# Performance work log

Hardware: AMD Instinct MI355X
Metric: run time of the kernel (lower is better)

Reference implementation:

```python
import jax, jax.numpy as jnp
import numpy as np

WS = 8  # window size (module uses window_sizes as a scalar)


def setup_inputs() -> dict:
    key = jax.random.key(0)
    ks = jax.random.split(key, 4)
    b, c, h, w = 4, 128, 256, 256
    x = jax.random.normal(ks[0], (b, c, h, w), jnp.float32)
    w_qkv = jax.random.normal(ks[1], (3 * c, c), jnp.float32) * (1.0 / np.sqrt(c))
    w_dw = jax.random.normal(ks[2], (3 * c, 1, 3, 3), jnp.float32) * (1.0 / 3.0)
    w_proj = jax.random.normal(ks[3], (c, c), jnp.float32) * (1.0 / np.sqrt(c))
    temperature = jnp.ones((1, 1, 1), jnp.float32)
    return {"x": x, "w_qkv": w_qkv, "w_dw": w_dw, "w_proj": w_proj,
            "temperature": temperature}


def _window(t, ws):
    # b c (h dh) (w dw) -> b (h w) (dh dw) c
    b, c, H, W = t.shape
    t = t.reshape(b, c, H // ws, ws, W // ws, ws)
    return t.transpose(0, 2, 4, 3, 5, 1).reshape(b, (H // ws) * (W // ws), ws * ws, c)


def _unwindow(t, ws, H, W):
    # b (h w) (dh dw) c -> b c (h dh) (w dw)
    b = t.shape[0]
    c = t.shape[-1]
    t = t.reshape(b, H // ws, W // ws, ws, ws, c)
    return t.transpose(0, 5, 1, 3, 2, 4).reshape(b, c, H, W)


def reference(x, w_qkv, w_dw, w_proj, temperature):
    b, c, H, W = x.shape
    ws = WS
    sh = -ws // 2  # = -(ws//2) for even ws, matching torch.roll shifts
    x_ = jnp.roll(x, (sh, sh), axis=(2, 3))
    # 1x1 conv c -> 3c
    qkv = jnp.einsum('oc,bchw->bohw', w_qkv, x_)
    # depthwise 3x3, padding 1
    qkv = jax.lax.conv_general_dilated(
        qkv, w_dw, window_strides=(1, 1), padding=[(1, 1), (1, 1)],
        dimension_numbers=('NCHW', 'OIHW', 'NCHW'), feature_group_count=3 * c)
    q, k, v = jnp.split(qkv, 3, axis=1)
    q = _window(q, ws)  # [b, nW, ws*ws, c]
    k = _window(k, ws)
    v = _window(v, ws)
    # L2-normalize along channel dim (torch F.normalize, eps=1e-12)
    q = q / jnp.maximum(jnp.linalg.norm(q, axis=-1, keepdims=True), 1e-12)
    k = k / jnp.maximum(jnp.linalg.norm(k, axis=-1, keepdims=True), 1e-12)
    # channel-wise attention: [b, nW, c, c]
    attn = jnp.einsum('bnpc,bnpd->bncd', q, k) * temperature.reshape(())
    attn = jax.nn.relu(attn)
    out = jnp.einsum('bnpc,bncd->bnpd', v, attn)  # [b, nW, ws*ws, c]
    out = _unwindow(out, ws, H, W)
    out = jnp.roll(out, (ws // 2, ws // 2), axis=(2, 3))
    y = jnp.einsum('oc,bchw->bohw', w_proj, out)
    return (y, attn)
```

## Files before the change

### kernel.cpp

```cpp
#include <hip/hip_runtime.h>
#include <hip/hip_bf16.h>

constexpr int NB = 4;
constexpr int CC = 128;
constexpr int HW = 65536;

using bf16x8 = __attribute__((ext_vector_type(8))) short;
using f32x4  = __attribute__((ext_vector_type(4))) float;

__device__ __forceinline__ unsigned short f2bf(float f) {
  unsigned u = __builtin_bit_cast(unsigned, f);
  u += 0x7FFFu + ((u >> 16) & 1u);
  return (unsigned short)(u >> 16);
}
__device__ __forceinline__ float bf2f(unsigned short s) {
  return __builtin_bit_cast(float, (unsigned)s << 16);
}

__device__ __forceinline__ void halo_decomp(int idx, int& ch, int& r, int& c) {
  ch = idx / 30;
  int rem = idx - ch * 30;
  r = rem / 3;
  c = rem - r * 3;
}
__device__ __forceinline__ uint4 halo_load_one(const __hip_bfloat16* __restrict__ base,
                                               int ih0, int iw0, int idx) {
  int ch, r, c;
  halo_decomp(idx, ch, r, c);
  int ii = ih0 - 1 + r, j0 = iw0 - 8 + c * 8;
  uint4 v = {0u, 0u, 0u, 0u};
  if ((unsigned)ii < 256u && (unsigned)j0 <= 248u)
    v = *(const uint4*)(base + (((size_t)ch) << 16) + (ii << 8) + j0);
  return v;
}
__device__ __forceinline__ void halo_store_one(unsigned short* __restrict__ halo,
                                               int idx, uint4 v) {
  int ch, r, c;
  halo_decomp(idx, ch, r, c);
  unsigned short* hrow = halo + ch * 168 + r * 16;
  if (c == 1) *(uint4*)hrow = v;
  else if (c == 0) hrow[9] = (unsigned short)(v.w >> 16);
  else hrow[8] = (unsigned short)(v.x & 0xFFFFu);
}

__device__ __forceinline__ void dw_row(const unsigned short* __restrict__ halo,
                                       const float* __restrict__ wd,
                                       int ch, int pr, float* __restrict__ outv) {
#pragma unroll
  for (int pc = 0; pc < 8; ++pc) outv[pc] = 0.f;
#pragma unroll
  for (int kr = 0; kr < 3; ++kr) {
    const unsigned short* hrow = halo + ch * 168 + (pr + kr) * 16;
    uint4 rw = *(const uint4*)hrow;
    float rv[10];
    rv[0] = bf2f((unsigned short)(rw.x & 0xFFFFu));
    rv[1] = bf2f((unsigned short)(rw.x >> 16));
    rv[2] = bf2f((unsigned short)(rw.y & 0xFFFFu));
    rv[3] = bf2f((unsigned short)(rw.y >> 16));
    rv[4] = bf2f((unsigned short)(rw.z & 0xFFFFu));
    rv[5] = bf2f((unsigned short)(rw.z >> 16));
    rv[6] = bf2f((unsigned short)(rw.w & 0xFFFFu));
    rv[7] = bf2f((unsigned short)(rw.w >> 16));
    rv[8] = bf2f(hrow[8]);
    rv[9] = bf2f(hrow[9]);
#pragma unroll
    for (int s = 0; s < 3; ++s) {
      float wv = wd[kr * 3 + s];
#pragma unroll
      for (int pc = 0; pc < 8; ++pc) {
        int m = pc + s - 1;
        float xv = (m < 0) ? rv[9] : rv[m];
        outv[pc] = fmaf(wv, xv, outv[pc]);
      }
    }
  }
}

__global__ __launch_bounds__(256) void k_qkv_mfma(const float* __restrict__ x,
                                                  const float* __restrict__ wq,
                                                  __hip_bfloat16* __restrict__ qkv) {
  __shared__ unsigned short x_s[128 * 136];

  int blk = blockIdx.x;
  int b = blk >> 9, i = (blk >> 1) & 255, jh = blk & 1;
  int j0 = jh << 7;
  int si = (i + 4) & 255;
  int t = threadIdx.x;

  {
    int c0 = (t & 63) << 1;
    int jb = (t >> 6) << 5;
    const float* xr0 = x + (((size_t)(b * CC + c0)) << 16) + (si << 8);
    const float* xr1 = xr0 + HW;
#pragma unroll
    for (int u = 0; u < 8; ++u) {
      int jj = jb + (u << 2);
      int sj = j0 + jj + 4;
      float v0[4], v1[4];
      if (sj + 3 <= 255) {
        *(float4*)v0 = *(const float4*)(xr0 + sj);
        *(float4*)v1 = *(const float4*)(xr1 + sj);
      } else {
#pragma unroll
        for (int e = 0; e < 4; ++e) {
          int s = (sj + e) & 255;
          v0[e] = xr0[s];
          v1[e] = xr1[s];
        }
      }
#pragma unroll
      for (int e = 0; e < 4; ++e) {
        unsigned pk = (unsigned)f2bf(v0[e]) | ((unsigned)f2bf(v1[e]) << 16);
        *(unsigned*)&x_s[(jj + e) * 136 + c0] = pk;
      }
    }
  }
  __syncthreads();

  int w = t >> 6;
  int lane = t & 63;
  int col = lane & 15;
  int kg = lane >> 4;

#pragma unroll 1
  for (int oi = 0; oi < 3; ++oi) {
    int m0 = oi * 128 + w * 32;
    bf16x8 afr[2][4];
#pragma unroll
    for (int mt = 0; mt < 2; ++mt) {
      const float* wr = wq + (m0 + mt * 16 + col) * CC + kg * 8;
#pragma unroll
      for (int ks = 0; ks < 4; ++ks) {
        float wa[4], wb[4];
        *(float4*)wa = *(const float4*)(wr + ks * 32);
        *(float4*)wb = *(const float4*)(wr + ks * 32 + 4);
        bf16x8 f;
#pragma unroll
        for (int e = 0; e < 4; ++e) {
          f[e] = (short)f2bf(wa[e]);
          f[e + 4] = (short)f2bf(wb[e]);
        }
        afr[mt][ks] = f;
      }
    }
#pragma unroll 1
    for (int n = 0; n < 8; ++n) {
      int px = n * 16 + col;
      f32x4 acc0 = {0.f, 0.f, 0.f, 0.f};
      f32x4 acc1 = {0.f, 0.f, 0.f, 0.f};
#pragma unroll
      for (int ks = 0; ks < 4; ++ks) {
        bf16x8 bfr = *(const bf16x8*)&x_s[px * 136 + ks * 32 + kg * 8];
        acc0 = __builtin_amdgcn_mfma_f32_16x16x32_bf16(afr[0][ks], bfr, acc0, 0, 0, 0);
        acc1 = __builtin_amdgcn_mfma_f32_16x16x32_bf16(afr[1][ks], bfr, acc1, 0, 0, 0);
      }
      int j = j0 + n * 16 + col;
#pragma unroll
      for (int r = 0; r < 4; ++r) {
        int och0 = m0 + kg * 4 + r;
        int och1 = m0 + 16 + kg * 4 + r;
        int g0 = och0 >> 7, c0 = och0 & 127;
        int g1 = och1 >> 7, c1 = och1 & 127;
        qkv[(((size_t)((g0 * NB + b) * CC + c0)) << 16) + (i << 8) + j] =
            __float2bfloat16(acc0[r]);
        qkv[(((size_t)((g1 * NB + b) * CC + c1)) << 16) + (i << 8) + j] =
            __float2bfloat16(acc1[r]);
      }
    }
  }
}

__global__ __launch_bounds__(256, 2) void k_fused(const __hip_bfloat16* __restrict__ qkv,
                                                  const float* __restrict__ wdw,
                                                  const float* __restrict__ temp_p,
                                                  const float* __restrict__ wp,
                                                  float* __restrict__ attn_out,
                                                  float* __restrict__ y) {
  __shared__ unsigned short halo_s[128 * 168];
  __shared__ unsigned short q_t[128][72];
  __shared__ unsigned short k_t[128][72];
  __shared__ float sumsq_s[2][64];

  int bid = blockIdx.x;
  int blk = ((bid & 7) << 9) + (bid >> 3);
  int b = blk >> 10, n = blk & 1023;
  int ih0 = (n >> 5) << 3, iw0 = (n & 31) << 3;
  int t = threadIdx.x;
  int ch_l = t & 15, grp = t >> 4;
  int pr = grp & 7, contrib = grp >> 3;
  float tau = temp_p[0];
  const __hip_bfloat16* qbase = qkv + (((size_t)(b * CC)) << 16);
  const __hip_bfloat16* kbase = qkv + (((size_t)((NB + b) * CC)) << 16);
  const __hip_bfloat16* vbase = qkv + (((size_t)((2 * NB + b) * CC)) << 16);

#pragma unroll
  for (int it = 0; it < 15; ++it) {
    int idx = it * 256 + t;
    halo_store_one(halo_s, idx, halo_load_one(qbase, ih0, iw0, idx));
  }
  __syncthreads();

  uint4 kpre[15];
#pragma unroll
  for (int it = 0; it < 15; ++it)
    kpre[it] = halo_load_one(kbase, ih0, iw0, it * 256 + t);

  float outv[4][8];
  float ssq[8];
#pragma unroll
  for (int pc = 0; pc < 8; ++pc) ssq[pc] = 0.f;
#pragma unroll
  for (int it = 0; it < 4; ++it) {
    int ch = ((contrib + 2 * it) << 4) + ch_l;
    float wd[9];
#pragma unroll
    for (int kk = 0; kk < 9; ++kk) wd[kk] = wdw[ch * 9 + kk];
    dw_row(halo_s, wd, ch, pr, outv[it]);
#pragma unroll
    for (int pc = 0; pc < 8; ++pc) ssq[pc] = fmaf(outv[it][pc], outv[it][pc], ssq[pc]);
  }
#pragma unroll
  for (int pc = 0; pc < 8; ++pc) {
    float s = ssq[pc];
    s += __shfl_xor(s, 1);
    s += __shfl_xor(s, 2);
    s += __shfl_xor(s, 4);
    s += __shfl_xor(s, 8);
    ssq[pc] = s;
  }
  if (ch_l == 0) {
#pragma unroll
    for (int pc = 0; pc < 8; ++pc) sumsq_s[contrib][pr * 8 + pc] = ssq[pc];
  }
  __syncthreads();

#pragma unroll
  for (int it = 0; it < 15; ++it) halo_store_one(halo_s, it * 256 + t, kpre[it]);
  {
    float psv[8];
#pragma unroll
    for (int pc = 0; pc < 8; ++pc) {
      float s = sumsq_s[0][pr * 8 + pc] + sumsq_s[1][pr * 8 + pc];
      psv[pc] = 1.f / fmaxf(sqrtf(s), 1e-12f);
    }
#pragma unroll
    for (int it = 0; it < 4; ++it) {
      int ch = ((contrib + 2 * it) << 4) + ch_l;
      unsigned short o8[8];
#pragma unroll
      for (int pc = 0; pc < 8; ++pc) o8[pc] = f2bf(outv[it][pc] * psv[pc]);
      *(uint4*)&q_t[ch][pr * 8] = *(const uint4*)o8;
    }
  }
  __syncthreads();

#pragma unroll
  for (int pc = 0; pc < 8; ++pc) ssq[pc] = 0.f;
#pragma unroll
  for (int it = 0; it < 4; ++it) {
    int ch = ((contrib + 2 * it) << 4) + ch_l;
    float wd[9];
#pragma unroll
    for (int kk = 0; kk < 9; ++kk) wd[kk] = wdw[(CC + ch) * 9 + kk];
    dw_row(halo_s, wd, ch, pr, outv[it]);
#pragma unroll
    for (int pc = 0; pc < 8; ++pc) ssq[pc] = fmaf(outv[it][pc], outv[it][pc], ssq[pc]);
  }
#pragma unroll
  for (int pc = 0; pc < 8; ++pc) {
    float s = ssq[pc];
    s += __shfl_xor(s, 1);
    s += __shfl_xor(s, 2);
    s += __shfl_xor(s, 4);
    s += __shfl_xor(s, 8);
    ssq[pc] = s;
  }
  if (ch_l == 0) {
#pragma unroll
    for (int pc = 0; pc < 8; ++pc) sumsq_s[contrib][pr * 8 + pc] = ssq[pc];
  }
  __syncthreads();

  {
    float psv[8];
#pragma unroll
    for (int pc = 0; pc < 8; ++pc) {
      float s = sumsq_s[0][pr * 8 + pc] + sumsq_s[1][pr * 8 + pc];
      psv[pc] = tau / fmaxf(sqrtf(s), 1e-12f);
    }
#pragma unroll
    for (int it = 0; it < 4; ++it) {
      int ch = ((contrib + 2 * it) << 4) + ch_l;
      unsigned short o8[8];
#pragma unroll
      for (int pc = 0; pc < 8; ++pc) o8[pc] = f2bf(outv[it][pc] * psv[pc]);
      *(uint4*)&k_t[ch][pr * 8] = *(const uint4*)o8;
    }
  }
  __syncthreads();

  uint4 vpre[15];
#pragma unroll
  for (int it = 0; it < 15; ++it)
    vpre[it] = halo_load_one(vbase, ih0, iw0, it * 256 + t);

  int wv = t >> 6, lane = t & 63;
  int col = lane & 15, kg = lane >> 4;
  int c0 = wv * 32;
  f32x4 pa0[8], pa1[8];
  {
    bf16x8 afr[2][2];
#pragma unroll
    for (int mt = 0; mt < 2; ++mt)
#pragma unroll
      for (int ks = 0; ks < 2; ++ks)
        afr[mt][ks] = *(const bf16x8*)&q_t[c0 + mt * 16 + col][ks * 32 + kg * 8];
    float* ao = attn_out + ((size_t)blk << 14);
#pragma unroll
    for (int dt = 0; dt < 8; ++dt) {
      bf16x8 b0 = *(const bf16x8*)&k_t[dt * 16 + col][kg * 8];
      bf16x8 b1 = *(const bf16x8*)&k_t[dt * 16 + col][32 + kg * 8];
      f32x4 a0 = {0.f, 0.f, 0.f, 0.f};
      f32x4 a1 = {0.f, 0.f, 0.f, 0.f};
      a0 = __builtin_amdgcn_mfma_f32_16x16x32_bf16(afr[0][0], b0, a0, 0, 0, 0);
      a0 = __builtin_amdgcn_mfma_f32_16x16x32_bf16(afr[0][1], b1, a0, 0, 0, 0);
      a1 = __builtin_amdgcn_mfma_f32_16x16x32_bf16(afr[1][0], b0, a1, 0, 0, 0);
      a1 = __builtin_amdgcn_mfma_f32_16x16x32_bf16(afr[1][1], b1, a1, 0, 0, 0);
#pragma unroll
      for (int r = 0; r < 4; ++r) {
        a0[r] = fmaxf(a0[r], 0.f);
        a1[r] = fmaxf(a1[r], 0.f);
        ao[((c0 + kg * 4 + r) << 7) + dt * 16 + col] = a0[r];
        ao[((c0 + 16 + kg * 4 + r) << 7) + dt * 16 + col] = a1[r];
      }
      pa0[dt] = a0;
      pa1[dt] = a1;
    }
  }
  __syncthreads();

#pragma unroll
  for (int it = 0; it < 15; ++it) halo_store_one(halo_s, it * 256 + t, vpre[it]);
  __syncthreads();

  unsigned short (*v_t)[136] = (unsigned short (*)[136])&q_t[0][0];
#pragma unroll
  for (int it = 0; it < 4; ++it) {
    int ch = ((contrib + 2 * it) << 4) + ch_l;
    float wd[9];
#pragma unroll
    for (int kk = 0; kk < 9; ++kk) wd[kk] = wdw[(2 * CC + ch) * 9 + kk];
    float vo[8];
    dw_row(halo_s, wd, ch, pr, vo);
#pragma unroll
    for (int pc = 0; pc < 8; ++pc) v_t[pr * 8 + pc][ch] = f2bf(vo[pc]);
  }
  __syncthreads();

  unsigned short (*a_t)[136] = (unsigned short (*)[136])halo_s;
#pragma unroll
  for (int dt = 0; dt < 8; ++dt)
#pragma unroll
    for (int r = 0; r < 4; ++r) {
      a_t[dt * 16 + col][c0 + kg * 4 + r] = f2bf(pa0[dt][r]);
      a_t[dt * 16 + col][c0 + 16 + kg * 4 + r] = f2bf(pa1[dt][r]);
    }
  __syncthreads();

  f32x4 pacc[8];
#pragma unroll
  for (int dt = 0; dt < 8; ++dt) pacc[dt] = {0.f, 0.f, 0.f, 0.f};
#pragma unroll
  for (int ks = 0; ks < 4; ++ks) {
    bf16x8 va = *(const bf16x8*)&v_t[wv * 16 + col][ks * 32 + kg * 8];
#pragma unroll
    for (int dt = 0; dt < 8; ++dt) {
      bf16x8 bf = *(const bf16x8*)&a_t[dt * 16 + col][ks * 32 + kg * 8];
      pacc[dt] = __builtin_amdgcn_mfma_f32_16x16x32_bf16(va, bf, pacc[dt], 0, 0, 0);
    }
  }
  __syncthreads();

  unsigned short (*po_t)[136] = (unsigned short (*)[136])halo_s;
#pragma unroll
  for (int dt = 0; dt < 8; ++dt)
#pragma unroll
    for (int r = 0; r < 4; ++r)
      po_t[wv * 16 + kg * 4 + r][dt * 16 + col] = f2bf(pacc[dt][r]);
  __syncthreads();

  {
    int p = wv * 16 + col;
    bf16x8 bfr[4];
#pragma unroll
    for (int ks = 0; ks < 4; ++ks)
      bfr[ks] = *(const bf16x8*)&po_t[p][ks * 32 + kg * 8];
    int i_f = (((n >> 5) << 3) + (p >> 3) + 4) & 255;
    int j_f = (((n & 31) << 3) + (p & 7) + 4) & 255;
    float* yp = y + (((size_t)b * CC) << 16) + (i_f << 8) + j_f;
#pragma unroll
    for (int mt = 0; mt < 8; ++mt) {
      bf16x8 afr[4];
      const float* wr = wp + (mt * 16 + col) * CC + kg * 8;
#pragma unroll
      for (int ks = 0; ks < 4; ++ks) {
        float wa[4], wb[4];
        *(float4*)wa = *(const float4*)(wr + ks * 32);
        *(float4*)wb = *(const float4*)(wr + ks * 32 + 4);
        bf16x8 f;
#pragma unroll
        for (int e = 0; e < 4; ++e) {
          f[e] = (short)f2bf(wa[e]);
          f[e + 4] = (short)f2bf(wb[e]);
        }
        afr[ks] = f;
      }
      f32x4 acc = {0.f, 0.f, 0.f, 0.f};
#pragma unroll
      for (int ks = 0; ks < 4; ++ks)
        acc = __builtin_amdgcn_mfma_f32_16x16x32_bf16(afr[ks], bfr[ks], acc, 0, 0, 0);
#pragma unroll
      for (int r = 0; r < 4; ++r) {
        int och = mt * 16 + kg * 4 + r;
        yp[(size_t)och << 16] = acc[r];
      }
    }
  }
}

extern "C" void kernel_launch(void* const* d_in, const int* in_sizes, int n_in,
                              void* d_out, int out_size, void* d_ws, size_t ws_size,
                              hipStream_t stream) {
  const float* x = (const float*)d_in[0];
  const float* w_qkv = (const float*)d_in[1];
  const float* w_dw = (const float*)d_in[2];
  const float* w_proj = (const float*)d_in[3];
  const float* temp = (const float*)d_in[4];
  float* y = (float*)d_out;
  float* attn = (float*)d_out + (size_t)NB * CC * HW;

  __hip_bfloat16* qkv = (__hip_bfloat16*)d_ws;

  k_qkv_mfma<<<2048, 256, 0, stream>>>(x, w_qkv, qkv);
  k_fused<<<4096, 256, 0, stream>>>(qkv, w_dw, temp, w_proj, attn, y);
}
```

Measured before the change: 646.6 us.

## Halve halo staging, swizzle LDS tiles, and raise occupancy to three blocks

The fused window-attention kernel now stages the depthwise-conv halo in 64-channel halves instead of all 128 channels. It overlaps the next half's global prefetch with the current half's depthwise compute and splits the V·attn MFMA loop into two K-halves. Shared memory is shrunk and the transposed q/k/v/attn tiles use XOR-swizzled layouts to avoid bank conflicts. Both kernels get launch bounds of 3 blocks per CU. In exchange the kernel needs more barriers and has a tighter register budget, which risks spills.

Result: slower. 965.7 us (+49.4%).

```diff
diff --git a/kernel.cpp b/kernel.cpp
--- a/kernel.cpp
+++ b/kernel.cpp
@@ -17,26 +17,25 @@
   return __builtin_bit_cast(float, (unsigned)s << 16);
 }
 
-__device__ __forceinline__ void halo_decomp(int idx, int& ch, int& r, int& c) {
-  ch = idx / 30;
+__device__ __forceinline__ int swz128(int row, int b) { return row * 128 + (b ^ ((row & 7) << 4)); }
+__device__ __forceinline__ int swz256(int row, int b) { return row * 256 + (b ^ ((row & 15) << 4)); }
+
+__device__ __forceinline__ uint4 hload(const __hip_bfloat16* __restrict__ base,
+                                       int ih0, int iw0, int idx) {
+  int ch = idx / 30;
   int rem = idx - ch * 30;
-  r = rem / 3;
-  c = rem - r * 3;
-}
-__device__ __forceinline__ uint4 halo_load_one(const __hip_bfloat16* __restrict__ base,
-                                               int ih0, int iw0, int idx) {
-  int ch, r, c;
-  halo_decomp(idx, ch, r, c);
+  int r = rem / 3, c = rem - r * 3;
   int ii = ih0 - 1 + r, j0 = iw0 - 8 + c * 8;
   uint4 v = {0u, 0u, 0u, 0u};
-  if ((unsigned)ii < 256u && (unsigned)j0 <= 248u)
+  if (idx < 1920 && (unsigned)ii < 256u && (unsigned)j0 <= 248u)
     v = *(const uint4*)(base + (((size_t)ch) << 16) + (ii << 8) + j0);
   return v;
 }
-__device__ __forceinline__ void halo_store_one(unsigned short* __restrict__ halo,
-                                               int idx, uint4 v) {
-  int ch, r, c;
-  halo_decomp(idx, ch, r, c);
+__device__ __forceinline__ void hstore(unsigned short* __restrict__ halo, int idx, uint4 v) {
+  if (idx >= 1920) return;
+  int ch = idx / 30;
+  int rem = idx - ch * 30;
+  int r = rem / 3, c = rem - r * 3;
   unsigned short* hrow = halo + ch * 168 + r * 16;
   if (c == 1) *(uint4*)hrow = v;
   else if (c == 0) hrow[9] = (unsigned short)(v.w >> 16);
@@ -45,12 +44,12 @@
 
 __device__ __forceinline__ void dw_row(const unsigned short* __restrict__ halo,
                                        const float* __restrict__ wd,
-                                       int ch, int pr, float* __restrict__ outv) {
+                                       int chl, int pr, float* __restrict__ outv) {
 #pragma unroll
   for (int pc = 0; pc < 8; ++pc) outv[pc] = 0.f;
 #pragma unroll
   for (int kr = 0; kr < 3; ++kr) {
-    const unsigned short* hrow = halo + ch * 168 + (pr + kr) * 16;
+    const unsigned short* hrow = halo + chl * 168 + (pr + kr) * 16;
     uint4 rw = *(const uint4*)hrow;
     float rv[10];
     rv[0] = bf2f((unsigned short)(rw.x & 0xFFFFu));
@@ -76,9 +75,30 @@
   }
 }
 
-__global__ __launch_bounds__(256) void k_qkv_mfma(const float* __restrict__ x,
-                                                  const float* __restrict__ wq,
-                                                  __hip_bfloat16* __restrict__ qkv) {
+template <bool SQ>
+__device__ __forceinline__ void dw_half(const unsigned short* __restrict__ halo,
+                                        const float* __restrict__ wdw_g,
+                                        int g0, int ch_l, int pr, int half,
+                                        float (*outv)[8], float* __restrict__ ssq) {
+#pragma unroll
+  for (int it = 0; it < 2; ++it) {
+    int chl = (g0 + 2 * it) * 16 + ch_l;
+    int chf = half * 64 + chl;
+    float wd[9];
+#pragma unroll
+    for (int kk = 0; kk < 9; ++kk) wd[kk] = wdw_g[chf * 9 + kk];
+    dw_row(halo, wd, chl, pr, outv[it]);
+    if (SQ) {
+#pragma unroll
+      for (int pc = 0; pc < 8; ++pc)
+        ssq[pc] = fmaf(outv[it][pc], outv[it][pc], ssq[pc]);
+    }
+  }
+}
+
+__global__ __launch_bounds__(256, 3) void k_qkv_mfma(const float* __restrict__ x,
+                                                     const float* __restrict__ wq,
+                                                     __hip_bfloat16* __restrict__ qkv) {
   __shared__ unsigned short x_s[128 * 136];
 
   int blk = blockIdx.x;
@@ -170,142 +190,116 @@
   }
 }
 
-__global__ __launch_bounds__(256, 2) void k_fused(const __hip_bfloat16* __restrict__ qkv,
+__global__ __launch_bounds__(256, 3) void k_fused(const __hip_bfloat16* __restrict__ qkv,
                                                   const float* __restrict__ wdw,
                                                   const float* __restrict__ temp_p,
                                                   const float* __restrict__ wp,
                                                   float* __restrict__ attn_out,
                                                   float* __restrict__ y) {
-  __shared__ unsigned short halo_s[128 * 168];
-  __shared__ unsigned short q_t[128][72];
-  __shared__ unsigned short k_t[128][72];
-  __shared__ float sumsq_s[2][64];
+  __shared__ __align__(16) char smem[54272];
+  unsigned short* halo = (unsigned short*)smem;
+  char* RB = smem + 21504;
+  char* RC = smem + 21504 + 16384;
 
   int bid = blockIdx.x;
   int blk = ((bid & 7) << 9) + (bid >> 3);
   int b = blk >> 10, n = blk & 1023;
   int ih0 = (n >> 5) << 3, iw0 = (n & 31) << 3;
   int t = threadIdx.x;
-  int ch_l = t & 15, grp = t >> 4;
-  int pr = grp & 7, contrib = grp >> 3;
+  int ch_l = t & 15;
+  int wv = t >> 6, lane = t & 63;
+  int col = lane & 15, kg = lane >> 4;
+  int giw = (t >> 4) & 3;
+  int pr = 2 * wv + (giw & 1);
+  int g0 = giw >> 1;
   float tau = temp_p[0];
-  const __hip_bfloat16* qbase = qkv + (((size_t)(b * CC)) << 16);
-  const __hip_bfloat16* kbase = qkv + (((size_t)((NB + b) * CC)) << 16);
-  const __hip_bfloat16* vbase = qkv + (((size_t)((2 * NB + b) * CC)) << 16);
-
-#pragma unroll
-  for (int it = 0; it < 15; ++it) {
-    int idx = it * 256 + t;
-    halo_store_one(halo_s, idx, halo_load_one(qbase, ih0, iw0, idx));
-  }
-  __syncthreads();
-
-  uint4 kpre[15];
-#pragma unroll
-  for (int it = 0; it < 15; ++it)
-    kpre[it] = halo_load_one(kbase, ih0, iw0, it * 256 + t);
-
+  const __hip_bfloat16* qb = qkv + (((size_t)(b * CC)) << 16);
+  const __hip_bfloat16* kb = qb + (((size_t)(NB * CC)) << 16);
+  const __hip_bfloat16* vb = qb + (((size_t)(2 * NB * CC)) << 16);
+  const size_t HALF = ((size_t)64) << 16;
+
+  uint4 pre[8];
   float outv[4][8];
   float ssq[8];
+
+#pragma unroll
+  for (int it = 0; it < 8; ++it) {
+    int idx = it * 256 + t;
+    hstore(halo, idx, hload(qb, ih0, iw0, idx));
+  }
+  __syncthreads();
+#pragma unroll
+  for (int it = 0; it < 8; ++it) pre[it] = hload(qb + HALF, ih0, iw0, it * 256 + t);
 #pragma unroll
   for (int pc = 0; pc < 8; ++pc) ssq[pc] = 0.f;
-#pragma unroll
-  for (int it = 0; it < 4; ++it) {
-    int ch = ((contrib + 2 * it) << 4) + ch_l;
-    float wd[9];
-#pragma unroll
-    for (int kk = 0; kk < 9; ++kk) wd[kk] = wdw[ch * 9 + kk];
-    dw_row(halo_s, wd, ch, pr, outv[it]);
-#pragma unroll
-    for (int pc = 0; pc < 8; ++pc) ssq[pc] = fmaf(outv[it][pc], outv[it][pc], ssq[pc]);
-  }
-#pragma unroll
-  for (int pc = 0; pc < 8; ++pc) {
-    float s = ssq[pc];
-    s += __shfl_xor(s, 1);
-    s += __shfl_xor(s, 2);
-    s += __shfl_xor(s, 4);
-    s += __shfl_xor(s, 8);
-    ssq[pc] = s;
-  }
-  if (ch_l == 0) {
-#pragma unroll
-    for (int pc = 0; pc < 8; ++pc) sumsq_s[contrib][pr * 8 + pc] = ssq[pc];
-  }
-  __syncthreads();
-
-#pragma unroll
-  for (int it = 0; it < 15; ++it) halo_store_one(halo_s, it * 256 + t, kpre[it]);
+  dw_half<true>(halo, wdw, g0, ch_l, pr, 0, &outv[0], ssq);
+  __syncthreads();
+#pragma unroll
+  for (int it = 0; it < 8; ++it) hstore(halo, it * 256 + t, pre[it]);
+  __syncthreads();
+#pragma unroll
+  for (int it = 0; it < 8; ++it) pre[it] = hload(kb, ih0, iw0, it * 256 + t);
+  dw_half<true>(halo, wdw, g0, ch_l, pr, 1, &outv[2], ssq);
   {
     float psv[8];
 #pragma unroll
     for (int pc = 0; pc < 8; ++pc) {
-      float s = sumsq_s[0][pr * 8 + pc] + sumsq_s[1][pr * 8 + pc];
+      float s = ssq[pc];
+      s += __shfl_xor(s, 1); s += __shfl_xor(s, 2);
+      s += __shfl_xor(s, 4); s += __shfl_xor(s, 8);
+      s += __shfl_xor(s, 32);
       psv[pc] = 1.f / fmaxf(sqrtf(s), 1e-12f);
     }
 #pragma unroll
-    for (int it = 0; it < 4; ++it) {
-      int ch = ((contrib + 2 * it) << 4) + ch_l;
+    for (int tk = 0; tk < 4; ++tk) {
+      int chf = (tk >> 1) * 64 + (g0 + 2 * (tk & 1)) * 16 + ch_l;
       unsigned short o8[8];
 #pragma unroll
-      for (int pc = 0; pc < 8; ++pc) o8[pc] = f2bf(outv[it][pc] * psv[pc]);
-      *(uint4*)&q_t[ch][pr * 8] = *(const uint4*)o8;
-    }
-  }
-  __syncthreads();
-
+      for (int pc = 0; pc < 8; ++pc) o8[pc] = f2bf(outv[tk][pc] * psv[pc]);
+      *(uint4*)(RB + swz128(chf, pr * 16)) = *(const uint4*)o8;
+    }
+  }
+  __syncthreads();
+#pragma unroll
+  for (int it = 0; it < 8; ++it) hstore(halo, it * 256 + t, pre[it]);
+  __syncthreads();
+#pragma unroll
+  for (int it = 0; it < 8; ++it) pre[it] = hload(kb + HALF, ih0, iw0, it * 256 + t);
 #pragma unroll
   for (int pc = 0; pc < 8; ++pc) ssq[pc] = 0.f;
-#pragma unroll
-  for (int it = 0; it < 4; ++it) {
-    int ch = ((contrib + 2 * it) << 4) + ch_l;
-    float wd[9];
-#pragma unroll
-    for (int kk = 0; kk < 9; ++kk) wd[kk] = wdw[(CC + ch) * 9 + kk];
-    dw_row(halo_s, wd, ch, pr, outv[it]);
-#pragma unroll
-    for (int pc = 0; pc < 8; ++pc) ssq[pc] = fmaf(outv[it][pc], outv[it][pc], ssq[pc]);
-  }
-#pragma unroll
-  for (int pc = 0; pc < 8; ++pc) {
-    float s = ssq[pc];
-    s += __shfl_xor(s, 1);
-    s += __shfl_xor(s, 2);
-    s += __shfl_xor(s, 4);
-    s += __shfl_xor(s, 8);
-    ssq[pc] = s;
-  }
-  if (ch_l == 0) {
-#pragma unroll
-    for (int pc = 0; pc < 8; ++pc) sumsq_s[contrib][pr * 8 + pc] = ssq[pc];
-  }
-  __syncthreads();
-
+  dw_half<true>(halo, wdw + CC * 9, g0, ch_l, pr, 0, &outv[0], ssq);
+  __syncthreads();
+#pragma unroll
+  for (int it = 0; it < 8; ++it) hstore(halo, it * 256 + t, pre[it]);
+  __syncthreads();
+#pragma unroll
+  for (int it = 0; it < 8; ++it) pre[it] = hload(vb, ih0, iw0, it * 256 + t);
+  dw_half<true>(halo, wdw + CC * 9, g0, ch_l, pr, 1, &outv[2], ssq);
   {
     float psv[8];
 #pragma unroll
     for (int pc = 0; pc < 8; ++pc) {
-      float s = sumsq_s[0][pr * 8 + pc] + sumsq_s[1][pr * 8 + pc];
+      float s = ssq[pc];
+      s += __shfl_xor(s, 1); s += __shfl_xor(s, 2);
+      s += __shfl_xor(s, 4); s += __shfl_xor(s, 8);
+      s += __shfl_xor(s, 32);
       psv[pc] = tau / fmaxf(sqrtf(s), 1e-12f);
     }
 #pragma unroll
-    for (int it = 0; it < 4; ++it) {
-      int ch = ((contrib + 2 * it) << 4) + ch_l;
+    for (int tk = 0; tk < 4; ++tk) {
+      int chf = (tk >> 1) * 64 + (g0 + 2 * (tk & 1)) * 16 + ch_l;
       unsigned short o8[8];
 #pragma unroll
-      for (int pc = 0; pc < 8; ++pc) o8[pc] = f2bf(outv[it][pc] * psv[pc]);
-      *(uint4*)&k_t[ch][pr * 8] = *(const uint4*)o8;
-    }
-  }
-  __syncthreads();
-
-  uint4 vpre[15];
-#pragma unroll
-  for (int it = 0; it < 15; ++it)
-    vpre[it] = halo_load_one(vbase, ih0, iw0, it * 256 + t);
-
-  int wv = t >> 6, lane = t & 63;
-  int col = lane & 15, kg = lane >> 4;
+      for (int pc = 0; pc < 8; ++pc) o8[pc] = f2bf(outv[tk][pc] * psv[pc]);
+      *(uint4*)(RC + swz128(chf, pr * 16)) = *(const uint4*)o8;
+    }
+  }
+  __syncthreads();
+#pragma unroll
+  for (int it = 0; it < 8; ++it) hstore(halo, it * 256 + t, pre[it]);
+  __syncthreads();
+#pragma unroll
+  for (int it = 0; it < 8; ++it) pre[it] = hload(vb + HALF, ih0, iw0, it * 256 + t);
   int c0 = wv * 32;
   f32x4 pa0[8], pa1[8];
   {
@@ -314,12 +308,12 @@
     for (int mt = 0; mt < 2; ++mt)
 #pragma unroll
       for (int ks = 0; ks < 2; ++ks)
-        afr[mt][ks] = *(const bf16x8*)&q_t[c0 + mt * 16 + col][ks * 32 + kg * 8];
+        afr[mt][ks] = *(const bf16x8*)(RB + swz128(c0 + mt * 16 + col, ks * 64 + kg * 16));
     float* ao = attn_out + ((size_t)blk << 14);
 #pragma unroll
     for (int dt = 0; dt < 8; ++dt) {
-      bf16x8 b0 = *(const bf16x8*)&k_t[dt * 16 + col][kg * 8];
-      bf16x8 b1 = *(const bf16x8*)&k_t[dt * 16 + col][32 + kg * 8];
+      bf16x8 b0 = *(const bf16x8*)(RC + swz128(dt * 16 + col, kg * 16));
+      bf16x8 b1 = *(const bf16x8*)(RC + swz128(dt * 16 + col, 64 + kg * 16));
       f32x4 a0 = {0.f, 0.f, 0.f, 0.f};
       f32x4 a1 = {0.f, 0.f, 0.f, 0.f};
       a0 = __builtin_amdgcn_mfma_f32_16x16x32_bf16(afr[0][0], b0, a0, 0, 0, 0);
@@ -338,63 +332,89 @@
     }
   }
   __syncthreads();
-
-#pragma unroll
-  for (int it = 0; it < 15; ++it) halo_store_one(halo_s, it * 256 + t, vpre[it]);
-  __syncthreads();
-
-  unsigned short (*v_t)[136] = (unsigned short (*)[136])&q_t[0][0];
-#pragma unroll
-  for (int it = 0; it < 4; ++it) {
-    int ch = ((contrib + 2 * it) << 4) + ch_l;
-    float wd[9];
-#pragma unroll
-    for (int kk = 0; kk < 9; ++kk) wd[kk] = wdw[(2 * CC + ch) * 9 + kk];
-    float vo[8];
-    dw_row(halo_s, wd, ch, pr, vo);
-#pragma unroll
-    for (int pc = 0; pc < 8; ++pc) v_t[pr * 8 + pc][ch] = f2bf(vo[pc]);
-  }
-  __syncthreads();
-
-  unsigned short (*a_t)[136] = (unsigned short (*)[136])halo_s;
+  {
+    float vo[2][8];
+    dw_half<false>(halo, wdw + 2 * CC * 9, g0, ch_l, pr, 0, vo, nullptr);
+#pragma unroll
+    for (int it = 0; it < 2; ++it) {
+      int chf = (g0 + 2 * it) * 16 + ch_l;
+#pragma unroll
+      for (int pc = 0; pc < 8; ++pc)
+        *(unsigned short*)(RB + swz256(pr * 8 + pc, chf * 2)) = f2bf(vo[it][pc]);
+    }
+  }
+  if (wv < 2) {
+#pragma unroll
+    for (int dt = 0; dt < 8; ++dt)
+#pragma unroll
+      for (int r = 0; r < 4; ++r) {
+        int d = dt * 16 + col;
+        *(unsigned short*)(RC + swz128(d, (c0 + kg * 4 + r) * 2)) = f2bf(pa0[dt][r]);
+        *(unsigned short*)(RC + swz128(d, (c0 + 16 + kg * 4 + r) * 2)) = f2bf(pa1[dt][r]);
+      }
+  }
+  __syncthreads();
+#pragma unroll
+  for (int it = 0; it < 8; ++it) hstore(halo, it * 256 + t, pre[it]);
+  f32x4 pacc[8];
+#pragma unroll
+  for (int dt = 0; dt < 8; ++dt) pacc[dt] = {0.f, 0.f, 0.f, 0.f};
+#pragma unroll
+  for (int ks = 0; ks < 2; ++ks) {
+    bf16x8 va = *(const bf16x8*)(RB + swz256(wv * 16 + col, ks * 64 + kg * 16));
+#pragma unroll
+    for (int dt = 0; dt < 8; ++dt) {
+      bf16x8 bf = *(const bf16x8*)(RC + swz128(dt * 16 + col, (ks & 1) * 64 + kg * 16));
+      pacc[dt] = __builtin_amdgcn_mfma_f32_16x16x32_bf16(va, bf, pacc[dt], 0, 0, 0);
+    }
+  }
+  __syncthreads();
+  {
+    float vo[2][8];
+    dw_half<false>(halo, wdw + 2 * CC * 9, g0, ch_l, pr, 1, vo, nullptr);
+#pragma unroll
+    for (int it = 0; it < 2; ++it) {
+      int chf = 64 + (g0 + 2 * it) * 16 + ch_l;
+#pragma unroll
+      for (int pc = 0; pc < 8; ++pc)
+        *(unsigned short*)(RB + swz256(pr * 8 + pc, chf * 2)) = f2bf(vo[it][pc]);
+    }
+  }
+  if (wv >= 2) {
+    int cl0 = c0 - 64;
+#pragma unroll
+    for (int dt = 0; dt < 8; ++dt)
+#pragma unroll
+      for (int r = 0; r < 4; ++r) {
+        int d = dt * 16 + col;
+        *(unsigned short*)(RC + swz128(d, (cl0 + kg * 4 + r) * 2)) = f2bf(pa0[dt][r]);
+        *(unsigned short*)(RC + swz128(d, (cl0 + 16 + kg * 4 + r) * 2)) = f2bf(pa1[dt][r]);
+      }
+  }
+  __syncthreads();
+#pragma unroll
+  for (int ks = 2; ks < 4; ++ks) {
+    bf16x8 va = *(const bf16x8*)(RB + swz256(wv * 16 + col, ks * 64 + kg * 16));
+#pragma unroll
+    for (int dt = 0; dt < 8; ++dt) {
+      bf16x8 bf = *(const bf16x8*)(RC + swz128(dt * 16 + col, (ks & 1) * 64 + kg * 16));
+      pacc[dt] = __builtin_amdgcn_mfma_f32_16x16x32_bf16(va, bf, pacc[dt], 0, 0, 0);
+    }
+  }
+  __syncthreads();
 #pragma unroll
   for (int dt = 0; dt < 8; ++dt)
 #pragma unroll
-    for (int r = 0; r < 4; ++r) {
-      a_t[dt * 16 + col][c0 + kg * 4 + r] = f2bf(pa0[dt][r]);
-      a_t[dt * 16 + col][c0 + 16 + kg * 4 + r] = f2bf(pa1[dt][r]);
-    }
-  __syncthreads();
-
-  f32x4 pacc[8];
-#pragma unroll
-  for (int dt = 0; dt < 8; ++dt) pacc[dt] = {0.f, 0.f, 0.f, 0.f};
-#pragma unroll
-  for (int ks = 0; ks < 4; ++ks) {
-    bf16x8 va = *(const bf16x8*)&v_t[wv * 16 + col][ks * 32 + kg * 8];
-#pragma unroll
-    for (int dt = 0; dt < 8; ++dt) {
-      bf16x8 bf = *(const bf16x8*)&a_t[dt * 16 + col][ks * 32 + kg * 8];
-      pacc[dt] = __builtin_amdgcn_mfma_f32_16x16x32_bf16(va, bf, pacc[dt], 0, 0, 0);
-    }
-  }
-  __syncthreads();
-
-  unsigned short (*po_t)[136] = (unsigned short (*)[136])halo_s;
-#pragma unroll
-  for (int dt = 0; dt < 8; ++dt)
-#pragma unroll
     for (int r = 0; r < 4; ++r)
-      po_t[wv * 16 + kg * 4 + r][dt * 16 + col] = f2bf(pacc[dt][r]);
-  __syncthreads();
-
+      *(unsigned short*)(RB + swz256(wv * 16 + kg * 4 + r, (dt * 16 + col) * 2)) =
+          f2bf(pacc[dt][r]);
+  __syncthreads();
   {
     int p = wv * 16 + col;
     bf16x8 bfr[4];
 #pragma unroll
     for (int ks = 0; ks < 4; ++ks)
-      bfr[ks] = *(const bf16x8*)&po_t[p][ks * 32 + kg * 8];
+      bfr[ks] = *(const bf16x8*)(RB + swz256(p, ks * 64 + kg * 16));
     int i_f = (((n >> 5) << 3) + (p >> 3) + 4) & 255;
     int j_f = (((n & 31) << 3) + (p & 7) + 4) & 255;
     float* yp = y + (((size_t)b * CC) << 16) + (i_f << 8) + j_f;
```

## Double fused-kernel block size to 512 threads and re-split per-thread work

Applied to the files above, without the earlier changes.

The fused window-attention kernel now launches 512 threads per block instead of 256. Each phase is re-partitioned to match: halo loads use 8 iterations instead of 15, each thread handles 2 channels in the depthwise stage, each wave handles 16 channel rows of attn, and the V·attn and projection GEMMs are split across point and output halves. This cuts per-thread register use (the prefetch buffers and accumulators shrink) and aims to raise the number of wavefronts available to hide memory latency. In exchange, the sum-of-squares reduction goes through 4 slices in shared memory, and LDS use per block is unchanged, which may limit how many blocks fit on a CU.

Result: slower. 696.5 us (+7.7%).

```diff
diff --git a/kernel.cpp b/kernel.cpp
--- a/kernel.cpp
+++ b/kernel.cpp
@@ -17,26 +17,22 @@
   return __builtin_bit_cast(float, (unsigned)s << 16);
 }
 
-__device__ __forceinline__ void halo_decomp(int idx, int& ch, int& r, int& c) {
-  ch = idx / 30;
+__device__ __forceinline__ uint4 hload(const __hip_bfloat16* __restrict__ base,
+                                       int ih0, int iw0, int idx) {
+  int ch = idx / 30;
   int rem = idx - ch * 30;
-  r = rem / 3;
-  c = rem - r * 3;
-}
-__device__ __forceinline__ uint4 halo_load_one(const __hip_bfloat16* __restrict__ base,
-                                               int ih0, int iw0, int idx) {
-  int ch, r, c;
-  halo_decomp(idx, ch, r, c);
+  int r = rem / 3, c = rem - r * 3;
   int ii = ih0 - 1 + r, j0 = iw0 - 8 + c * 8;
   uint4 v = {0u, 0u, 0u, 0u};
-  if ((unsigned)ii < 256u && (unsigned)j0 <= 248u)
+  if (idx < 3840 && (unsigned)ii < 256u && (unsigned)j0 <= 248u)
     v = *(const uint4*)(base + (((size_t)ch) << 16) + (ii << 8) + j0);
   return v;
 }
-__device__ __forceinline__ void halo_store_one(unsigned short* __restrict__ halo,
-                                               int idx, uint4 v) {
-  int ch, r, c;
-  halo_decomp(idx, ch, r, c);
+__device__ __forceinline__ void hstore(unsigned short* __restrict__ halo, int idx, uint4 v) {
+  if (idx >= 3840) return;
+  int ch = idx / 30;
+  int rem = idx - ch * 30;
+  int r = rem / 3, c = rem - r * 3;
   unsigned short* hrow = halo + ch * 168 + r * 16;
   if (c == 1) *(uint4*)hrow = v;
   else if (c == 0) hrow[9] = (unsigned short)(v.w >> 16);
@@ -170,16 +166,16 @@
   }
 }
 
-__global__ __launch_bounds__(256, 2) void k_fused(const __hip_bfloat16* __restrict__ qkv,
-                                                  const float* __restrict__ wdw,
-                                                  const float* __restrict__ temp_p,
-                                                  const float* __restrict__ wp,
-                                                  float* __restrict__ attn_out,
-                                                  float* __restrict__ y) {
+__global__ __launch_bounds__(512) void k_fused(const __hip_bfloat16* __restrict__ qkv,
+                                               const float* __restrict__ wdw,
+                                               const float* __restrict__ temp_p,
+                                               const float* __restrict__ wp,
+                                               float* __restrict__ attn_out,
+                                               float* __restrict__ y) {
   __shared__ unsigned short halo_s[128 * 168];
   __shared__ unsigned short q_t[128][72];
   __shared__ unsigned short k_t[128][72];
-  __shared__ float sumsq_s[2][64];
+  __shared__ float sumsq_s[4][64];
 
   int bid = blockIdx.x;
   int blk = ((bid & 7) << 9) + (bid >> 3);
@@ -188,30 +184,31 @@
   int t = threadIdx.x;
   int ch_l = t & 15, grp = t >> 4;
   int pr = grp & 7, contrib = grp >> 3;
+  int wv = t >> 6, lane = t & 63;
+  int col = lane & 15, kg = lane >> 4;
   float tau = temp_p[0];
-  const __hip_bfloat16* qbase = qkv + (((size_t)(b * CC)) << 16);
-  const __hip_bfloat16* kbase = qkv + (((size_t)((NB + b) * CC)) << 16);
-  const __hip_bfloat16* vbase = qkv + (((size_t)((2 * NB + b) * CC)) << 16);
-
-#pragma unroll
-  for (int it = 0; it < 15; ++it) {
-    int idx = it * 256 + t;
-    halo_store_one(halo_s, idx, halo_load_one(qbase, ih0, iw0, idx));
-  }
-  __syncthreads();
-
-  uint4 kpre[15];
-#pragma unroll
-  for (int it = 0; it < 15; ++it)
-    kpre[it] = halo_load_one(kbase, ih0, iw0, it * 256 + t);
-
-  float outv[4][8];
+  const __hip_bfloat16* qb = qkv + (((size_t)(b * CC)) << 16);
+  const __hip_bfloat16* kb = qb + (((size_t)(NB * CC)) << 16);
+  const __hip_bfloat16* vb = qb + (((size_t)(2 * NB * CC)) << 16);
+
+  uint4 pre[8];
+  float outv[2][8];
   float ssq[8];
+
+#pragma unroll
+  for (int it = 0; it < 8; ++it) {
+    int idx = it * 512 + t;
+    hstore(halo_s, idx, hload(qb, ih0, iw0, idx));
+  }
+  __syncthreads();
+
+#pragma unroll
+  for (int it = 0; it < 8; ++it) pre[it] = hload(kb, ih0, iw0, it * 512 + t);
 #pragma unroll
   for (int pc = 0; pc < 8; ++pc) ssq[pc] = 0.f;
 #pragma unroll
-  for (int it = 0; it < 4; ++it) {
-    int ch = ((contrib + 2 * it) << 4) + ch_l;
+  for (int it = 0; it < 2; ++it) {
+    int ch = ((contrib + 4 * it) << 4) + ch_l;
     float wd[9];
 #pragma unroll
     for (int kk = 0; kk < 9; ++kk) wd[kk] = wdw[ch * 9 + kk];
@@ -222,10 +219,8 @@
 #pragma unroll
   for (int pc = 0; pc < 8; ++pc) {
     float s = ssq[pc];
-    s += __shfl_xor(s, 1);
-    s += __shfl_xor(s, 2);
-    s += __shfl_xor(s, 4);
-    s += __shfl_xor(s, 8);
+    s += __shfl_xor(s, 1); s += __shfl_xor(s, 2);
+    s += __shfl_xor(s, 4); s += __shfl_xor(s, 8);
     ssq[pc] = s;
   }
   if (ch_l == 0) {
@@ -235,17 +230,18 @@
   __syncthreads();
 
 #pragma unroll
-  for (int it = 0; it < 15; ++it) halo_store_one(halo_s, it * 256 + t, kpre[it]);
+  for (int it = 0; it < 8; ++it) hstore(halo_s, it * 512 + t, pre[it]);
   {
     float psv[8];
 #pragma unroll
     for (int pc = 0; pc < 8; ++pc) {
-      float s = sumsq_s[0][pr * 8 + pc] + sumsq_s[1][pr * 8 + pc];
+      float s = sumsq_s[0][pr * 8 + pc] + sumsq_s[1][pr * 8 + pc] +
+                sumsq_s[2][pr * 8 + pc] + sumsq_s[3][pr * 8 + pc];
       psv[pc] = 1.f / fmaxf(sqrtf(s), 1e-12f);
     }
 #pragma unroll
-    for (int it = 0; it < 4; ++it) {
-      int ch = ((contrib + 2 * it) << 4) + ch_l;
+    for (int it = 0; it < 2; ++it) {
+      int ch = ((contrib + 4 * it) << 4) + ch_l;
       unsigned short o8[8];
 #pragma unroll
       for (int pc = 0; pc < 8; ++pc) o8[pc] = f2bf(outv[it][pc] * psv[pc]);
@@ -257,8 +253,8 @@
 #pragma unroll
   for (int pc = 0; pc < 8; ++pc) ssq[pc] = 0.f;
 #pragma unroll
-  for (int it = 0; it < 4; ++it) {
-    int ch = ((contrib + 2 * it) << 4) + ch_l;
+  for (int it = 0; it < 2; ++it) {
+    int ch = ((contrib + 4 * it) << 4) + ch_l;
     float wd[9];
 #pragma unroll
     for (int kk = 0; kk < 9; ++kk) wd[kk] = wdw[(CC + ch) * 9 + kk];
@@ -269,10 +265,8 @@
 #pragma unroll
   for (int pc = 0; pc < 8; ++pc) {
     float s = ssq[pc];
-    s += __shfl_xor(s, 1);
-    s += __shfl_xor(s, 2);
-    s += __shfl_xor(s, 4);
-    s += __shfl_xor(s, 8);
+    s += __shfl_xor(s, 1); s += __shfl_xor(s, 2);
+    s += __shfl_xor(s, 4); s += __shfl_xor(s, 8);
     ssq[pc] = s;
   }
   if (ch_l == 0) {
@@ -285,12 +279,13 @@
     float psv[8];
 #pragma unroll
     for (int pc = 0; pc < 8; ++pc) {
-      float s = sumsq_s[0][pr * 8 + pc] + sumsq_s[1][pr * 8 + pc];
+      float s = sumsq_s[0][pr * 8 + pc] + sumsq_s[1][pr * 8 + pc] +
+                sumsq_s[2][pr * 8 + pc] + sumsq_s[3][pr * 8 + pc];
       psv[pc] = tau / fmaxf(sqrtf(s), 1e-12f);
     }
 #pragma unroll
-    for (int it = 0; it < 4; ++it) {
-      int ch = ((contrib + 2 * it) << 4) + ch_l;
+    for (int it = 0; it < 2; ++it) {
+      int ch = ((contrib + 4 * it) << 4) + ch_l;
       unsigned short o8[8];
 #pragma unroll
       for (int pc = 0; pc < 8; ++pc) o8[pc] = f2bf(outv[it][pc] * psv[pc]);
@@ -299,54 +294,41 @@
   }
   __syncthreads();
 
-  uint4 vpre[15];
-#pragma unroll
-  for (int it = 0; it < 15; ++it)
-    vpre[it] = halo_load_one(vbase, ih0, iw0, it * 256 + t);
-
-  int wv = t >> 6, lane = t & 63;
-  int col = lane & 15, kg = lane >> 4;
-  int c0 = wv * 32;
-  f32x4 pa0[8], pa1[8];
+#pragma unroll
+  for (int it = 0; it < 8; ++it) pre[it] = hload(vb, ih0, iw0, it * 512 + t);
+  int c0 = wv * 16;
+  f32x4 pa[8];
   {
-    bf16x8 afr[2][2];
-#pragma unroll
-    for (int mt = 0; mt < 2; ++mt)
-#pragma unroll
-      for (int ks = 0; ks < 2; ++ks)
-        afr[mt][ks] = *(const bf16x8*)&q_t[c0 + mt * 16 + col][ks * 32 + kg * 8];
+    bf16x8 afr[2];
+#pragma unroll
+    for (int ks = 0; ks < 2; ++ks)
+      afr[ks] = *(const bf16x8*)&q_t[c0 + col][ks * 32 + kg * 8];
     float* ao = attn_out + ((size_t)blk << 14);
 #pragma unroll
     for (int dt = 0; dt < 8; ++dt) {
       bf16x8 b0 = *(const bf16x8*)&k_t[dt * 16 + col][kg * 8];
       bf16x8 b1 = *(const bf16x8*)&k_t[dt * 16 + col][32 + kg * 8];
       f32x4 a0 = {0.f, 0.f, 0.f, 0.f};
-      f32x4 a1 = {0.f, 0.f, 0.f, 0.f};
-      a0 = __builtin_amdgcn_mfma_f32_16x16x32_bf16(afr[0][0], b0, a0, 0, 0, 0);
-      a0 = __builtin_amdgcn_mfma_f32_16x16x32_bf16(afr[0][1], b1, a0, 0, 0, 0);
-      a1 = __builtin_amdgcn_mfma_f32_16x16x32_bf16(afr[1][0], b0, a1, 0, 0, 0);
-      a1 = __builtin_amdgcn_mfma_f32_16x16x32_bf16(afr[1][1], b1, a1, 0, 0, 0);
+      a0 = __builtin_amdgcn_mfma_f32_16x16x32_bf16(afr[0], b0, a0, 0, 0, 0);
+      a0 = __builtin_amdgcn_mfma_f32_16x16x32_bf16(afr[1], b1, a0, 0, 0, 0);
 #pragma unroll
       for (int r = 0; r < 4; ++r) {
         a0[r] = fmaxf(a0[r], 0.f);
-        a1[r] = fmaxf(a1[r], 0.f);
         ao[((c0 + kg * 4 + r) << 7) + dt * 16 + col] = a0[r];
-        ao[((c0 + 16 + kg * 4 + r) << 7) + dt * 16 + col] = a1[r];
-      }
-      pa0[dt] = a0;
-      pa1[dt] = a1;
-    }
-  }
-  __syncthreads();
-
-#pragma unroll
-  for (int it = 0; it < 15; ++it) halo_store_one(halo_s, it * 256 + t, vpre[it]);
+      }
+      pa[dt] = a0;
+    }
+  }
+  __syncthreads();
+
+#pragma unroll
+  for (int it = 0; it < 8; ++it) hstore(halo_s, it * 512 + t, pre[it]);
   __syncthreads();
 
   unsigned short (*v_t)[136] = (unsigned short (*)[136])&q_t[0][0];
 #pragma unroll
-  for (int it = 0; it < 4; ++it) {
-    int ch = ((contrib + 2 * it) << 4) + ch_l;
+  for (int it = 0; it < 2; ++it) {
+    int ch = ((contrib + 4 * it) << 4) + ch_l;
     float wd[9];
 #pragma unroll
     for (int kk = 0; kk < 9; ++kk) wd[kk] = wdw[(2 * CC + ch) * 9 + kk];
@@ -361,21 +343,20 @@
 #pragma unroll
   for (int dt = 0; dt < 8; ++dt)
 #pragma unroll
-    for (int r = 0; r < 4; ++r) {
-      a_t[dt * 16 + col][c0 + kg * 4 + r] = f2bf(pa0[dt][r]);
-      a_t[dt * 16 + col][c0 + 16 + kg * 4 + r] = f2bf(pa1[dt][r]);
-    }
-  __syncthreads();
-
-  f32x4 pacc[8];
-#pragma unroll
-  for (int dt = 0; dt < 8; ++dt) pacc[dt] = {0.f, 0.f, 0.f, 0.f};
+    for (int r = 0; r < 4; ++r)
+      a_t[dt * 16 + col][c0 + kg * 4 + r] = f2bf(pa[dt][r]);
+  __syncthreads();
+
+  int pt = wv & 3, dh = wv >> 2;
+  f32x4 pacc[4];
+#pragma unroll
+  for (int dt = 0; dt < 4; ++dt) pacc[dt] = {0.f, 0.f, 0.f, 0.f};
 #pragma unroll
   for (int ks = 0; ks < 4; ++ks) {
-    bf16x8 va = *(const bf16x8*)&v_t[wv * 16 + col][ks * 32 + kg * 8];
-#pragma unroll
-    for (int dt = 0; dt < 8; ++dt) {
-      bf16x8 bf = *(const bf16x8*)&a_t[dt * 16 + col][ks * 32 + kg * 8];
+    bf16x8 va = *(const bf16x8*)&v_t[pt * 16 + col][ks * 32 + kg * 8];
+#pragma unroll
+    for (int dt = 0; dt < 4; ++dt) {
+      bf16x8 bf = *(const bf16x8*)&a_t[dh * 64 + dt * 16 + col][ks * 32 + kg * 8];
       pacc[dt] = __builtin_amdgcn_mfma_f32_16x16x32_bf16(va, bf, pacc[dt], 0, 0, 0);
     }
   }
@@ -383,14 +364,14 @@
 
   unsigned short (*po_t)[136] = (unsigned short (*)[136])halo_s;
 #pragma unroll
-  for (int dt = 0; dt < 8; ++dt)
+  for (int dt = 0; dt < 4; ++dt)
 #pragma unroll
     for (int r = 0; r < 4; ++r)
-      po_t[wv * 16 + kg * 4 + r][dt * 16 + col] = f2bf(pacc[dt][r]);
+      po_t[pt * 16 + kg * 4 + r][dh * 64 + dt * 16 + col] = f2bf(pacc[dt][r]);
   __syncthreads();
 
   {
-    int p = wv * 16 + col;
+    int p = pt * 16 + col;
     bf16x8 bfr[4];
 #pragma unroll
     for (int ks = 0; ks < 4; ++ks)
@@ -399,9 +380,9 @@
     int j_f = (((n & 31) << 3) + (p & 7) + 4) & 255;
     float* yp = y + (((size_t)b * CC) << 16) + (i_f << 8) + j_f;
 #pragma unroll
-    for (int mt = 0; mt < 8; ++mt) {
+    for (int mt = 0; mt < 4; ++mt) {
       bf16x8 afr[4];
-      const float* wr = wp + (mt * 16 + col) * CC + kg * 8;
+      const float* wr = wp + (dh * 64 + mt * 16 + col) * CC + kg * 8;
 #pragma unroll
       for (int ks = 0; ks < 4; ++ks) {
         float wa[4], wb[4];
@@ -421,7 +402,7 @@
         acc = __builtin_amdgcn_mfma_f32_16x16x32_bf16(afr[ks], bfr[ks], acc, 0, 0, 0);
 #pragma unroll
       for (int r = 0; r < 4; ++r) {
-        int och = mt * 16 + kg * 4 + r;
+        int och = dh * 64 + mt * 16 + kg * 4 + r;
         yp[(size_t)och << 16] = acc[r];
       }
     }
@@ -442,5 +423,5 @@
   __hip_bfloat16* qkv = (__hip_bfloat16*)d_ws;
 
   k_qkv_mfma<<<2048, 256, 0, stream>>>(x, w_qkv, qkv);
-  k_fused<<<4096, 256, 0, stream>>>(qkv, w_dw, temp, w_proj, attn, y);
-}
+  k_fused<<<4096, 512, 0, stream>>>(qkv, w_dw, temp, w_proj, attn, y);
+}
```
